# Kernel tuning notes

Measured on AMD Instinct MI355X. Metric: run time of the kernel, lower is better.

The kernel has to match this reference:

```python
import jax, jax.numpy as jnp
import numpy as np

B, TE, TD, D, U = 8, 256, 256, 256, 256


def setup_inputs() -> dict:
    key = jax.random.key(0)
    k1, k2, k3, k4, k5 = jax.random.split(key, 5)
    glorot = lambda k, shape: jax.random.uniform(
        k, shape, jnp.float32,
        -np.sqrt(6.0 / (shape[0] + shape[1])), np.sqrt(6.0 / (shape[0] + shape[1])))
    return {
        "en_seq": jax.random.normal(k1, (B, TE, D), jnp.float32),
        "de_seq": jax.random.normal(k2, (B, TD, D), jnp.float32),
        "w_en": glorot(k3, (D, U)),
        "w_de": glorot(k4, (D, U)),
        "nu": glorot(k5, (U, 1)),
    }


def reference(en_seq, de_seq, w_en, w_de, nu):
    # Additive co-attention scores.
    ae = jnp.einsum('bte,eu->btu', en_seq, w_en)          # (B, Te, U)
    ad = jnp.einsum('bsd,du->bsu', de_seq, w_de)          # (B, Td, U)
    # co_m[b, td, te, u] = ae[b, te, u] + ad[b, td, u]  (matches K.repeat / repeat_elements layout)
    co = jnp.tanh(ad[:, :, None, :] + ae[:, None, :, :])  # (B, Td, Te, U)
    mu = jnp.einsum('bstu,ul->bst', co, nu)               # (B, Td, Te)
    alphas = jax.nn.softmax(mu, axis=-1)                  # softmax over en time
    max_mu = jnp.max(mu, axis=-1)                         # (B, Td)
    max_alphas = jax.nn.softmax(max_mu, axis=-1)          # softmax over de time
    h_hat = jnp.sum(de_seq * max_alphas[..., None], axis=1)  # (B, Dd)
    sum_en = jnp.einsum('bst,bte->bse', alphas, en_seq)      # (B, Td, De)
    output = jnp.concatenate(
        [de_seq, sum_en, de_seq * sum_en, de_seq * h_hat[:, None, :]], axis=-1)
    return output  # (B, Td, 4*D)
```

## Files before the change

kernel.cpp:

```cpp
#include <hip/hip_runtime.h>

#define B_   8
#define TE_  256
#define TD_  256
#define D_   256
#define U_   256

#define AE_OFF    0
#define AD_OFF    524288
#define MU_OFF    1048576
#define MAXMU_OFF 1572864
#define HH_OFF    1574912

__device__ __forceinline__ float fexp2(float x) {
#if __has_builtin(__builtin_amdgcn_exp2f)
  return __builtin_amdgcn_exp2f(x);
#else
  return exp2f(x);
#endif
}
__device__ __forceinline__ float frcp(float x) {
#if __has_builtin(__builtin_amdgcn_rcpf)
  return __builtin_amdgcn_rcpf(x);
#else
  return 1.0f / x;
#endif
}

#define LOG2E_F 1.4426950408889634f
#define TWO_LOG2E_F 2.8853900817779268f

__global__ __launch_bounds__(256) void coatt_k1_proj(
    const float* __restrict__ en, const float* __restrict__ de,
    const float* __restrict__ w_en, const float* __restrict__ w_de,
    float* __restrict__ ws) {
  const int which = blockIdx.z;
  const float* __restrict__ A = which ? de : en;
  const float* __restrict__ W = which ? w_de : w_en;
  float* __restrict__ out = ws + (which ? AD_OFF : AE_OFF);
  const int rowBase = blockIdx.y * 64;
  const int colBase = blockIdx.x * 64;
  __shared__ float As[16][68];
  __shared__ float Bs[16][68];
  const int tid = threadIdx.x;
  const int tx = tid & 15, ty = tid >> 4;
  float acc[4][4] = {};
  for (int k0 = 0; k0 < D_; k0 += 16) {
    {
      const int r = tid >> 2;
      const int c = (tid & 3) * 4;
      const float4 a4 = *(const float4*)&A[(rowBase + r) * D_ + k0 + c];
      As[c + 0][r] = a4.x; As[c + 1][r] = a4.y;
      As[c + 2][r] = a4.z; As[c + 3][r] = a4.w;
      const int kk = tid >> 4;
      const int cc = (tid & 15) * 4;
      *(float4*)&Bs[kk][cc] = *(const float4*)&W[(k0 + kk) * U_ + colBase + cc];
    }
    __syncthreads();
#pragma unroll
    for (int k = 0; k < 16; ++k) {
      float av[4], bv[4];
      *(float4*)av = *(const float4*)&As[k][ty * 4];
      *(float4*)bv = *(const float4*)&Bs[k][tx * 4];
#pragma unroll
      for (int i = 0; i < 4; ++i)
#pragma unroll
        for (int j = 0; j < 4; ++j)
          acc[i][j] = fmaf(av[i], bv[j], acc[i][j]);
    }
    __syncthreads();
  }
#pragma unroll
  for (int i = 0; i < 4; ++i) {
    float4 o;
    o.x = acc[i][0] * TWO_LOG2E_F; o.y = acc[i][1] * TWO_LOG2E_F;
    o.z = acc[i][2] * TWO_LOG2E_F; o.w = acc[i][3] * TWO_LOG2E_F;
    *(float4*)&out[(rowBase + ty * 4 + i) * U_ + colBase + tx * 4] = o;
  }
}

__global__ __launch_bounds__(256) void coatt_k2_mu(
    const float* __restrict__ nu, float* __restrict__ ws) {
  const float* __restrict__ ae = ws + AE_OFF;
  const float* __restrict__ ad = ws + AD_OFF;
  float* __restrict__ mu = ws + MU_OFF;
  const int b = blockIdx.z;
  const int sBase = blockIdx.y * 32;
  const int tBase = blockIdx.x * 32;
  __shared__ float ADs[32][20];
  __shared__ float AEs[32][20];
  __shared__ float NUs[16];
  const int tid = threadIdx.x;
  const int tx = tid & 15;
  const int sy = tid >> 4;
  float acc00 = 0.f, acc01 = 0.f, acc10 = 0.f, acc11 = 0.f;
  for (int u0 = 0; u0 < U_; u0 += 16) {
    {
      const int r = (tid & 127) >> 2;
      const int c = (tid & 3) * 4;
      if (tid < 128)
        *(float4*)&ADs[r][c] = *(const float4*)&ad[(b * TD_ + sBase + r) * U_ + u0 + c];
      else
        *(float4*)&AEs[r][c] = *(const float4*)&ae[(b * TE_ + tBase + r) * U_ + u0 + c];
      if (tid < 4) {
        const float4 n4 = *(const float4*)&nu[u0 + tid * 4];
        NUs[tid * 4 + 0] = -2.0f * n4.x;
        NUs[tid * 4 + 1] = -2.0f * n4.y;
        NUs[tid * 4 + 2] = -2.0f * n4.z;
        NUs[tid * 4 + 3] = -2.0f * n4.w;
      }
    }
    __syncthreads();
    const float4* A0 = (const float4*)&ADs[sy][0];
    const float4* A1 = (const float4*)&ADs[sy + 16][0];
    const float4* E0 = (const float4*)&AEs[tx][0];
    const float4* E1 = (const float4*)&AEs[tx + 16][0];
    const float4* N4 = (const float4*)&NUs[0];
#pragma unroll
    for (int q = 0; q < 4; ++q) {
      float a0v[4], a1v[4], e0v[4], e1v[4], nv[4];
      *(float4*)a0v = A0[q];
      *(float4*)a1v = A1[q];
      *(float4*)e0v = E0[q];
      *(float4*)e1v = E1[q];
      *(float4*)nv  = N4[q];
#pragma unroll
      for (int u = 0; u < 4; ++u) {
        const float r00 = frcp(fexp2(a0v[u] + e0v[u]) + 1.0f);
        const float r01 = frcp(fexp2(a0v[u] + e1v[u]) + 1.0f);
        const float r10 = frcp(fexp2(a1v[u] + e0v[u]) + 1.0f);
        const float r11 = frcp(fexp2(a1v[u] + e1v[u]) + 1.0f);
        acc00 = fmaf(nv[u], r00, acc00);
        acc01 = fmaf(nv[u], r01, acc01);
        acc10 = fmaf(nv[u], r10, acc10);
        acc11 = fmaf(nv[u], r11, acc11);
      }
    }
    __syncthreads();
  }
  const int s0 = sBase + sy, s1 = s0 + 16;
  const int t0 = tBase + tx, t1 = t0 + 16;
  mu[(b * TD_ + s0) * TE_ + t0] = acc00;
  mu[(b * TD_ + s0) * TE_ + t1] = acc01;
  mu[(b * TD_ + s1) * TE_ + t0] = acc10;
  mu[(b * TD_ + s1) * TE_ + t1] = acc11;
}

__global__ __launch_bounds__(256) void coatt_k3_softmax(float* __restrict__ ws) {
  float* __restrict__ mu = ws + MU_OFF;
  float* __restrict__ maxmu = ws + MAXMU_OFF;
  const int row = blockIdx.x;
  const int tid = threadIdx.x;
  __shared__ float red[256];
  const float v = mu[row * TE_ + tid];
  red[tid] = v;
  __syncthreads();
  for (int w = 128; w > 0; w >>= 1) {
    if (tid < w) red[tid] = fmaxf(red[tid], red[tid + w]);
    __syncthreads();
  }
  const float m = red[0];
  __syncthreads();
  const float e = fexp2((v - m) * LOG2E_F);
  red[tid] = e;
  __syncthreads();
  for (int w = 128; w > 0; w >>= 1) {
    if (tid < w) red[tid] += red[tid + w];
    __syncthreads();
  }
  const float inv = frcp(red[0]);
  mu[row * TE_ + tid] = e * inv;
  if (tid == 0) maxmu[row] = m;
}

__global__ __launch_bounds__(256) void coatt_k4_hhat(
    const float* __restrict__ de, float* __restrict__ ws) {
  const float* __restrict__ maxmu = ws + MAXMU_OFF;
  float* __restrict__ hhat = ws + HH_OFF;
  const int b = blockIdx.y;
  const int dBase = blockIdx.x * 32;
  const int tid = threadIdx.x;
  __shared__ float red[256];
  __shared__ float malpha[256];
  const float v = maxmu[b * TD_ + tid];
  red[tid] = v;
  __syncthreads();
  for (int w = 128; w > 0; w >>= 1) {
    if (tid < w) red[tid] = fmaxf(red[tid], red[tid + w]);
    __syncthreads();
  }
  const float m = red[0];
  __syncthreads();
  const float e = fexp2((v - m) * LOG2E_F);
  red[tid] = e;
  __syncthreads();
  for (int w = 128; w > 0; w >>= 1) {
    if (tid < w) red[tid] += red[tid + w];
    __syncthreads();
  }
  malpha[tid] = e * frcp(red[0]);
  __syncthreads();
  const int dl = tid & 31, sg = tid >> 5;
  float acc = 0.f;
  for (int s = sg * 32; s < sg * 32 + 32; ++s)
    acc = fmaf(de[(b * TD_ + s) * D_ + dBase + dl], malpha[s], acc);
  red[tid] = acc;
  __syncthreads();
  if (tid < 32) {
    float t = red[tid];
#pragma unroll
    for (int g = 1; g < 8; ++g) t += red[g * 32 + tid];
    hhat[b * D_ + dBase + tid] = t;
  }
}

__global__ __launch_bounds__(256) void coatt_k5_out(
    const float* __restrict__ en, const float* __restrict__ de,
    const float* __restrict__ ws, float* __restrict__ out) {
  const float* __restrict__ alphas = ws + MU_OFF;
  const float* __restrict__ hhat = ws + HH_OFF;
  const int b = blockIdx.z;
  const int sBase = blockIdx.y * 32;
  const int eBase = blockIdx.x * 32;
  __shared__ float As[16][36];
  __shared__ float Bs[16][36];
  const int tid = threadIdx.x;
  const int tx = tid & 15, sy = tid >> 4;
  float acc[2][2] = {};
  for (int k0 = 0; k0 < TE_; k0 += 16) {
    if (tid < 128) {
      const int r = tid >> 2, c = (tid & 3) * 4;
      const float4 a4 = *(const float4*)&alphas[(b * TD_ + sBase + r) * TE_ + k0 + c];
      As[c + 0][r] = a4.x; As[c + 1][r] = a4.y;
      As[c + 2][r] = a4.z; As[c + 3][r] = a4.w;
    } else {
      const int id = tid & 127;
      const int kk = id >> 3, cc = (id & 7) * 4;
      *(float4*)&Bs[kk][cc] = *(const float4*)&en[(b * TE_ + k0 + kk) * D_ + eBase + cc];
    }
    __syncthreads();
#pragma unroll
    for (int k = 0; k < 16; ++k) {
      const float2 a2 = *(const float2*)&As[k][sy * 2];
      const float2 b2 = *(const float2*)&Bs[k][tx * 2];
      acc[0][0] = fmaf(a2.x, b2.x, acc[0][0]);
      acc[0][1] = fmaf(a2.x, b2.y, acc[0][1]);
      acc[1][0] = fmaf(a2.y, b2.x, acc[1][0]);
      acc[1][1] = fmaf(a2.y, b2.y, acc[1][1]);
    }
    __syncthreads();
  }
  const int e0 = eBase + tx * 2;
  const float2 hh = *(const float2*)&hhat[b * D_ + e0];
#pragma unroll
  for (int i = 0; i < 2; ++i) {
    const int s = sBase + sy * 2 + i;
    const float2 d2 = *(const float2*)&de[(b * TD_ + s) * D_ + e0];
    float* o = out + (size_t)(b * TD_ + s) * (4 * D_);
    float2 se; se.x = acc[i][0]; se.y = acc[i][1];
    *(float2*)&o[e0] = d2;
    *(float2*)&o[D_ + e0] = se;
    float2 p; p.x = d2.x * se.x; p.y = d2.y * se.y;
    *(float2*)&o[2 * D_ + e0] = p;
    float2 q; q.x = d2.x * hh.x; q.y = d2.y * hh.y;
    *(float2*)&o[3 * D_ + e0] = q;
  }
}

extern "C" void kernel_launch(void* const* d_in, const int* in_sizes, int n_in,
                              void* d_out, int out_size, void* d_ws, size_t ws_size,
                              hipStream_t stream) {
  (void)in_sizes; (void)n_in; (void)out_size; (void)ws_size;
  const float* en   = (const float*)d_in[0];
  const float* de   = (const float*)d_in[1];
  const float* w_en = (const float*)d_in[2];
  const float* w_de = (const float*)d_in[3];
  const float* nu   = (const float*)d_in[4];
  float* out = (float*)d_out;
  float* ws  = (float*)d_ws;

  coatt_k1_proj<<<dim3(4, 32, 2), 256, 0, stream>>>(en, de, w_en, w_de, ws);
  coatt_k2_mu<<<dim3(8, 8, 8), 256, 0, stream>>>(nu, ws);
  coatt_k3_softmax<<<dim3(2048), 256, 0, stream>>>(ws);
  coatt_k4_hhat<<<dim3(8, 8), 256, 0, stream>>>(de, ws);
  coatt_k5_out<<<dim3(8, 8, 8), 256, 0, stream>>>(en, de, ws, out);
}
```

Before: 135.0 us.

## Factor exp out of pairwise tanh and use wave-shuffle softmax

Uses exp2(a+e) = exp2(a)*exp2(e) to move the exponential into the projection kernel, so each pairwise tanh term in the mu kernel becomes one FMA plus a reciprocal instead of an exp, an add and a reciprocal. This removes the dominant transcendental work in the O(B*Td*Te*U) loop. Separately, the softmax kernel now handles one row per 64-lane wave with float4 loads and shuffle reductions instead of shared-memory tree reductions. The exponent product can overflow to inf for large projections, which still gives the right tanh limit via rcp(inf)=0, and the change slightly alters rounding.

```diff
diff --git a/kernel.cpp b/kernel.cpp
--- a/kernel.cpp
+++ b/kernel.cpp
@@ -73,8 +73,10 @@
 #pragma unroll
   for (int i = 0; i < 4; ++i) {
     float4 o;
-    o.x = acc[i][0] * TWO_LOG2E_F; o.y = acc[i][1] * TWO_LOG2E_F;
-    o.z = acc[i][2] * TWO_LOG2E_F; o.w = acc[i][3] * TWO_LOG2E_F;
+    o.x = fexp2(acc[i][0] * TWO_LOG2E_F);
+    o.y = fexp2(acc[i][1] * TWO_LOG2E_F);
+    o.z = fexp2(acc[i][2] * TWO_LOG2E_F);
+    o.w = fexp2(acc[i][3] * TWO_LOG2E_F);
     *(float4*)&out[(rowBase + ty * 4 + i) * U_ + colBase + tx * 4] = o;
   }
 }
@@ -126,10 +128,10 @@
       *(float4*)nv  = N4[q];
 #pragma unroll
       for (int u = 0; u < 4; ++u) {
-        const float r00 = frcp(fexp2(a0v[u] + e0v[u]) + 1.0f);
-        const float r01 = frcp(fexp2(a0v[u] + e1v[u]) + 1.0f);
-        const float r10 = frcp(fexp2(a1v[u] + e0v[u]) + 1.0f);
-        const float r11 = frcp(fexp2(a1v[u] + e1v[u]) + 1.0f);
+        const float r00 = frcp(fmaf(a0v[u], e0v[u], 1.0f));
+        const float r01 = frcp(fmaf(a0v[u], e1v[u], 1.0f));
+        const float r10 = frcp(fmaf(a1v[u], e0v[u], 1.0f));
+        const float r11 = frcp(fmaf(a1v[u], e1v[u], 1.0f));
         acc00 = fmaf(nv[u], r00, acc00);
         acc01 = fmaf(nv[u], r01, acc01);
         acc10 = fmaf(nv[u], r10, acc10);
@@ -149,28 +151,25 @@
 __global__ __launch_bounds__(256) void coatt_k3_softmax(float* __restrict__ ws) {
   float* __restrict__ mu = ws + MU_OFF;
   float* __restrict__ maxmu = ws + MAXMU_OFF;
-  const int row = blockIdx.x;
-  const int tid = threadIdx.x;
-  __shared__ float red[256];
-  const float v = mu[row * TE_ + tid];
-  red[tid] = v;
-  __syncthreads();
-  for (int w = 128; w > 0; w >>= 1) {
-    if (tid < w) red[tid] = fmaxf(red[tid], red[tid + w]);
-    __syncthreads();
-  }
-  const float m = red[0];
-  __syncthreads();
-  const float e = fexp2((v - m) * LOG2E_F);
-  red[tid] = e;
-  __syncthreads();
-  for (int w = 128; w > 0; w >>= 1) {
-    if (tid < w) red[tid] += red[tid + w];
-    __syncthreads();
-  }
-  const float inv = frcp(red[0]);
-  mu[row * TE_ + tid] = e * inv;
-  if (tid == 0) maxmu[row] = m;
+  const int tid = threadIdx.x;
+  const int wave = tid >> 6, lane = tid & 63;
+  const int row = blockIdx.x * 4 + wave;
+  float4 v = *(const float4*)&mu[row * TE_ + lane * 4];
+  float m = fmaxf(fmaxf(v.x, v.y), fmaxf(v.z, v.w));
+#pragma unroll
+  for (int off = 32; off > 0; off >>= 1) m = fmaxf(m, __shfl_xor(m, off));
+  float4 e;
+  e.x = fexp2((v.x - m) * LOG2E_F);
+  e.y = fexp2((v.y - m) * LOG2E_F);
+  e.z = fexp2((v.z - m) * LOG2E_F);
+  e.w = fexp2((v.w - m) * LOG2E_F);
+  float s = (e.x + e.y) + (e.z + e.w);
+#pragma unroll
+  for (int off = 32; off > 0; off >>= 1) s += __shfl_xor(s, off);
+  const float inv = frcp(s);
+  e.x *= inv; e.y *= inv; e.z *= inv; e.w *= inv;
+  *(float4*)&mu[row * TE_ + lane * 4] = e;
+  if (lane == 0) maxmu[row] = m;
 }
 
 __global__ __launch_bounds__(256) void coatt_k4_hhat(
@@ -281,7 +280,7 @@
 
   coatt_k1_proj<<<dim3(4, 32, 2), 256, 0, stream>>>(en, de, w_en, w_de, ws);
   coatt_k2_mu<<<dim3(8, 8, 8), 256, 0, stream>>>(nu, ws);
-  coatt_k3_softmax<<<dim3(2048), 256, 0, stream>>>(ws);
+  coatt_k3_softmax<<<dim3(512), 256, 0, stream>>>(ws);
   coatt_k4_hhat<<<dim3(8, 8), 256, 0, stream>>>(de, ws);
   coatt_k5_out<<<dim3(8, 8, 8), 256, 0, stream>>>(en, de, ws, out);
 }
```

Result: faster. 122.6 us (-9.2%).
